# Performance work log

Hardware: AMD Instinct MI355X
Metric: run time of the kernel (lower is better)

Reference implementation:

```python
import jax, jax.numpy as jnp
import numpy as np

B, N, L = 1, 128, 256
D_MSA, D_HID, D_PAIR = 256, 32, 128
EPS = 1e-5


def setup_inputs() -> dict:
    key = jax.random.key(0)
    ks = jax.random.split(key, 8)
    msa = jax.random.normal(ks[0], (B, N, L, D_MSA), dtype=jnp.float32)
    pair = jax.random.normal(ks[1], (B, L, L, D_PAIR), dtype=jnp.float32)
    symmids = jax.random.randint(ks[2], (1,), 0, 1, dtype=jnp.int64)
    symmsub = jax.random.randint(ks[3], (1,), 0, 1, dtype=jnp.int64)
    # learned params (lecun-normal-ish scale = 1/sqrt(fan_in))
    ln_gamma = jnp.ones((D_MSA,), jnp.float32)
    ln_beta = jnp.zeros((D_MSA,), jnp.float32)
    w_left = jax.random.normal(ks[4], (D_MSA, D_HID), jnp.float32) / np.sqrt(D_MSA)
    b_left = jnp.zeros((D_HID,), jnp.float32)
    w_right = jax.random.normal(ks[5], (D_MSA, D_HID), jnp.float32) / np.sqrt(D_MSA)
    b_right = jnp.zeros((D_HID,), jnp.float32)
    w_out = jax.random.normal(ks[6], (D_HID * D_HID, D_PAIR), jnp.float32) / np.sqrt(D_HID * D_HID)
    b_out = jnp.zeros((D_PAIR,), jnp.float32)
    return {
        "msa": msa, "pair": pair, "symmids": symmids, "symmsub": symmsub,
        "ln_gamma": ln_gamma, "ln_beta": ln_beta,
        "w_left": w_left, "b_left": b_left,
        "w_right": w_right, "b_right": b_right,
        "w_out": w_out, "b_out": b_out,
    }


def reference(msa, pair, symmids, symmsub, ln_gamma, ln_beta,
              w_left, b_left, w_right, b_right, w_out, b_out):
    b, n, l, _ = msa.shape
    # LayerNorm over d_msa (biased variance, matching torch)
    mu = jnp.mean(msa, axis=-1, keepdims=True)
    var = jnp.mean(jnp.square(msa - mu), axis=-1, keepdims=True)
    x = (msa - mu) * jax.lax.rsqrt(var + EPS) * ln_gamma + ln_beta
    left = x @ w_left + b_left                       # [b, n, l, d_h]
    right = (x @ w_right + b_right) / float(n)       # [b, n, l, d_h]
    # outer product, reduced over MSA (s) dim -> [b, l, m, d_h, d_h]
    out = jnp.einsum('bsli,bsmj->blmij', left, right).reshape(b, l, l, -1)
    out = out @ w_out + b_out                        # [b, l, l, d_pair]
    return pair + out
```

## Files before the change

kernel.cpp:

```cpp
#include <hip/hip_runtime.h>


typedef float v4f __attribute__((ext_vector_type(4)));
typedef short v8s __attribute__((ext_vector_type(8)));

static __device__ inline unsigned short f2bf(float x) {
    unsigned int u = __builtin_bit_cast(unsigned int, x);
    return (unsigned short)((u + 0x7fffu + ((u >> 16) & 1u)) >> 16);
}

__global__ __launch_bounds__(256) void k_prep(const float* __restrict__ w_out,
                                              const float* __restrict__ wl,
                                              const float* __restrict__ wr,
                                              unsigned short* __restrict__ w2,
                                              unsigned short* __restrict__ wTg) {
    const int b = blockIdx.x, t = threadIdx.x;
    unsigned short tmp[8];
    if (b < 64) {
        int tgt = b * 2048 + t * 8;
        int p = (tgt >> 6) & 127;
        int ck = tgt >> 13, kc0 = tgt & 63;
        for (int e = 0; e < 8; ++e) {
            int kp = ck * 64 + kc0 + e;
            int j1 = (kp >> 9) & 1, qd = (kp >> 7) & 3, lp = (kp >> 3) & 15;
            int i1 = (kp >> 2) & 1, r = kp & 3;
            int ii = i1 * 16 + qd * 4 + r, jj = j1 * 16 + lp;
            tmp[e] = f2bf(w_out[(ii * 32 + jj) * 128 + p]);
        }
        *(uint4*)&w2[tgt] = *(const uint4*)tmp;
    } else {
        int tgt = (b - 64) * 2048 + t * 8;
        int c = tgt >> 8, d0 = tgt & 255;
        const float* src = (c < 32) ? wl : wr;
        int cc = c & 31;
        for (int e = 0; e < 8; ++e) tmp[e] = f2bf(src[(d0 + e) * 32 + cc]);
        *(uint4*)&wTg[tgt] = *(const uint4*)tmp;
    }
}

__global__ __launch_bounds__(256) void k_lnproj(
    const float* __restrict__ msa, const float* __restrict__ gamma, const float* __restrict__ beta,
    const unsigned short* __restrict__ wTg, const float* __restrict__ bl, const float* __restrict__ br,
    unsigned short* __restrict__ leftT, unsigned short* __restrict__ rightT) {
    __shared__ unsigned short xb[32 * 264];
    __shared__ unsigned short wlds[64 * 264];
    __shared__ unsigned short outT[64 * 40];

    const int t = threadIdx.x, lane = t & 63, w = t >> 6;
    const int l = blockIdx.x, s0 = blockIdx.y * 32;
    const int quad = lane >> 4, l15 = lane & 15;

    for (int it = 0; it < 8; ++it) {
        int idx = it * 2048 + t * 8;
        *(uint4*)&wlds[(idx >> 8) * 264 + (idx & 255)] = *(const uint4*)&wTg[idx];
    }

    float4 g4 = *(const float4*)&gamma[lane * 4];
    float4 be4 = *(const float4*)&beta[lane * 4];
    float4 vr[8]; float s1[8], s2[8];
    for (int r = 0; r < 8; ++r) {
        const float* row = msa + (size_t)((s0 + w * 8 + r) * 256 + l) * 256;
        vr[r] = *(const float4*)&row[lane * 4];
    }
    for (int r = 0; r < 8; ++r) {
        float4 v = vr[r];
        s1[r] = v.x + v.y + v.z + v.w;
        s2[r] = v.x * v.x + v.y * v.y + v.z * v.z + v.w * v.w;
    }
    for (int o = 32; o > 0; o >>= 1)
        for (int r = 0; r < 8; ++r) { s1[r] += __shfl_xor(s1[r], o); s2[r] += __shfl_xor(s2[r], o); }
    for (int r = 0; r < 8; ++r) {
        float mu = s1[r] * (1.f / 256);
        float rs = rsqrtf(s2[r] * (1.f / 256) - mu * mu + 1e-5f);
        float4 v = vr[r];
        ushort4 xs;
        xs.x = f2bf((v.x - mu) * rs * g4.x + be4.x);
        xs.y = f2bf((v.y - mu) * rs * g4.y + be4.y);
        xs.z = f2bf((v.z - mu) * rs * g4.z + be4.z);
        xs.w = f2bf((v.w - mu) * rs * g4.w + be4.w);
        *(ushort4*)&xb[(w * 8 + r) * 264 + lane * 4] = xs;
    }
    __syncthreads();

    const int mt = w >> 1, ntb = (w & 1) * 2;
    v4f acc[2] = {};
    const int frow = (mt * 16 + l15) * 264;
    for (int ks = 0; ks < 8; ++ks) {
        int k = ks * 32 + quad * 8;
        v8s a = *(const v8s*)&xb[frow + k];
        v8s b0 = *(const v8s*)&wlds[(ntb * 16 + l15) * 264 + k];
        v8s b1 = *(const v8s*)&wlds[((ntb + 1) * 16 + l15) * 264 + k];
        acc[0] = __builtin_amdgcn_mfma_f32_16x16x32_bf16(a, b0, acc[0], 0, 0, 0);
        acc[1] = __builtin_amdgcn_mfma_f32_16x16x32_bf16(a, b1, acc[1], 0, 0, 0);
    }

    for (int tn = 0; tn < 2; ++tn) {
        int c = (ntb + tn) * 16 + l15;
        float bias = c < 32 ? bl[c] : br[c - 32];
        float scale = c < 32 ? 1.f : (1.f / 128);
        for (int r = 0; r < 4; ++r)
            outT[c * 40 + mt * 16 + quad * 4 + r] = f2bf((acc[tn][r] + bias) * scale);
    }
    __syncthreads();

    {
        int c = t >> 2, q = t & 3;
        uint4 vv = *(const uint4*)&outT[c * 40 + q * 8];
        int kh = s0 >> 6;
        int g = ((s0 & 32) >> 3) + q;
        int g2 = g ^ (c & 7);
        unsigned short* dst = (c < 32) ? (leftT + l * 4096 + c * 128)
                                       : (rightT + l * 4096 + (c - 32) * 128);
        *(uint4*)&dst[kh * 64 + g2 * 8] = vv;
    }
}

__global__ __launch_bounds__(256) void k_outer(
    const unsigned short* __restrict__ leftT, const unsigned short* __restrict__ rightT,
    const unsigned short* __restrict__ w2g, const float* __restrict__ bout,
    const float* __restrict__ pairIn, float* __restrict__ out) {
    __shared__ alignas(16) unsigned short smem[24576];
    unsigned short* Ah = smem;
    unsigned short* Bh = smem + 8192;
    unsigned short* Obuf = smem;
    unsigned short* wbuf = smem + 16384;

    const int t = threadIdx.x, lane = t & 63, w = t >> 6;
    const int l0 = blockIdx.x * 4, m0 = blockIdx.y * 4;
    const int wm = w & 1, wn = w >> 1;
    const int quad = lane >> 4, l15 = lane & 15;

    const unsigned short* Asrc = leftT + l0 * 4096;
    const unsigned short* Bsrc = rightT + m0 * 4096;

    v4f acc[4][4] = {};
    for (int kh = 0; kh < 2; ++kh) {
        __syncthreads();
        for (int it = 0; it < 4; ++it) {
            int el = (it * 256 + t) * 8;
            int m = el >> 6, off = el & 63;
            *(uint4*)&Ah[m * 64 + off] = *(const uint4*)&Asrc[m * 128 + kh * 64 + off];
            *(uint4*)&Bh[m * 64 + off] = *(const uint4*)&Bsrc[m * 128 + kh * 64 + off];
        }
        __syncthreads();
        for (int ks = 0; ks < 2; ++ks) {
            int g = ks * 4 + quad;
            v8s a[4], bb[4];
            for (int i = 0; i < 4; ++i)
                a[i] = *(const v8s*)&Ah[(wm * 64 + i * 16 + l15) * 64 + ((g ^ (l15 & 7)) << 3)];
            for (int j = 0; j < 4; ++j)
                bb[j] = *(const v8s*)&Bh[(wn * 64 + j * 16 + l15) * 64 + ((g ^ (l15 & 7)) << 3)];
            for (int i = 0; i < 4; ++i)
                for (int j = 0; j < 4; ++j)
                    acc[i][j] = __builtin_amdgcn_mfma_f32_16x16x32_bf16(a[i], bb[j], acc[i][j], 0, 0, 0);
        }
    }
    __syncthreads();

    for (int a2 = 0; a2 < 2; ++a2)
        for (int b2 = 0; b2 < 2; ++b2) {
            int pr = (wm * 2 + a2) * 4 + wn * 2 + b2;
            for (int j1 = 0; j1 < 2; ++j1) {
                unsigned short tmp8[8];
                for (int i1 = 0; i1 < 2; ++i1)
                    for (int r = 0; r < 4; ++r)
                        tmp8[i1 * 4 + r] = f2bf(acc[a2 * 2 + i1][b2 * 2 + j1][r]);
                int pg = (j1 * 64 + lane) ^ (pr & 7);
                *(uint4*)&Obuf[pr * 1024 + pg * 8] = *(const uint4*)tmp8;
            }
        }
    __syncthreads();

    v4f acc2[2] = {};
    {
        const unsigned short* wsrc = w2g + w * 2048;
        unsigned short* wb = wbuf + w * 2048;
        int wa[4];
        uint4 pf[4];
        for (int u = 0; u < 4; ++u) {
            int g2 = (lane & 1) * 4 + u;
            wa[u] = (lane >> 1) * 64 + ((g2 ^ ((lane >> 1) & 7)) << 3);
            pf[u] = *(const uint4*)&wsrc[lane * 32 + u * 8];
        }
        for (int ck = 0; ck < 16; ++ck) {
            for (int u = 0; u < 4; ++u) *(uint4*)&wb[wa[u]] = pf[u];
            if (ck < 15)
                for (int u = 0; u < 4; ++u)
                    pf[u] = *(const uint4*)&wsrc[(ck + 1) * 8192 + lane * 32 + u * 8];
            for (int inner = 0; inner < 2; ++inner) {
                int g = ck * 8 + inner * 4 + quad;
                v8s a = *(const v8s*)&Obuf[l15 * 1024 + ((g ^ (l15 & 7)) << 3)];
                for (int tt = 0; tt < 2; ++tt) {
                    v8s bfr = *(const v8s*)&wb[(tt * 16 + l15) * 64 + (((inner * 4 + quad) ^ (l15 & 7)) << 3)];
                    acc2[tt] = __builtin_amdgcn_mfma_f32_16x16x32_bf16(a, bfr, acc2[tt], 0, 0, 0);
                }
            }
        }
    }

    for (int tt = 0; tt < 2; ++tt) {
        int p = (w * 2 + tt) * 16 + l15;
        float bo = bout[p];
        for (int r = 0; r < 4; ++r) {
            int pr = quad * 4 + r;
            int dl = pr >> 2, dm = pr & 3;
            size_t idx = (size_t)((l0 + dl) * 256 + (m0 + dm)) * 128 + p;
            out[idx] = pairIn[idx] + bo + acc2[tt][r];
        }
    }
}

extern "C" void kernel_launch(void* const* d_in, const int* in_sizes, int n_in,
                              void* d_out, int out_size, void* d_ws, size_t ws_size,
                              hipStream_t stream) {
    const float* msa   = (const float*)d_in[0];
    const float* pairI = (const float*)d_in[1];
    const float* gamma = (const float*)d_in[4];
    const float* beta  = (const float*)d_in[5];
    const float* wl    = (const float*)d_in[6];
    const float* bl    = (const float*)d_in[7];
    const float* wr    = (const float*)d_in[8];
    const float* br    = (const float*)d_in[9];
    const float* wout  = (const float*)d_in[10];
    const float* bout  = (const float*)d_in[11];
    float* out = (float*)d_out;

    unsigned short* leftT  = (unsigned short*)d_ws;
    unsigned short* rightT = leftT + 256 * 32 * 128;
    unsigned short* w2     = rightT + 256 * 32 * 128;
    unsigned short* wTg    = w2 + 131072;

    k_prep<<<dim3(72), 256, 0, stream>>>(wout, wl, wr, w2, wTg);
    k_lnproj<<<dim3(256, 4), 256, 0, stream>>>(msa, gamma, beta, wTg, bl, br, leftT, rightT);
    k_outer<<<dim3(64, 64), 256, 0, stream>>>(leftT, rightT, w2, bout, pairI, out);
}
```

Baseline: 200.7 us.

## Load weight fragments directly from global and use async global-to-LDS copies

In the LN+projection kernel, the staging of the projection weights through shared memory is removed, and MFMA B-fragments are read straight from global (L2-cached) memory. In the outer-product kernel, the A/B tile loads use global_load_lds to bypass registers. The w_out fragments are double-buffered in registers instead of being staged through LDS, which cuts LDS use from 48KB to 32KB and may raise occupancy. Risks: more global load latency exposed in the inner loops, and any mismatch between the w2g layout and the new direct fragment indexing.

```diff
diff --git a/kernel.cpp b/kernel.cpp
--- a/kernel.cpp
+++ b/kernel.cpp
@@ -7,6 +7,12 @@
 static __device__ inline unsigned short f2bf(float x) {
     unsigned int u = __builtin_bit_cast(unsigned int, x);
     return (unsigned short)((u + 0x7fffu + ((u >> 16) & 1u)) >> 16);
+}
+
+static __device__ inline void glds16(const void* g, void* l) {
+    __builtin_amdgcn_global_load_lds(
+        (const __attribute__((address_space(1))) unsigned int*)g,
+        (__attribute__((address_space(3))) unsigned int*)l, 16, 0, 0);
 }
 
 __global__ __launch_bounds__(256) void k_prep(const float* __restrict__ w_out,
@@ -43,17 +49,11 @@
     const unsigned short* __restrict__ wTg, const float* __restrict__ bl, const float* __restrict__ br,
     unsigned short* __restrict__ leftT, unsigned short* __restrict__ rightT) {
     __shared__ unsigned short xb[32 * 264];
-    __shared__ unsigned short wlds[64 * 264];
     __shared__ unsigned short outT[64 * 40];
 
     const int t = threadIdx.x, lane = t & 63, w = t >> 6;
     const int l = blockIdx.x, s0 = blockIdx.y * 32;
     const int quad = lane >> 4, l15 = lane & 15;
-
-    for (int it = 0; it < 8; ++it) {
-        int idx = it * 2048 + t * 8;
-        *(uint4*)&wlds[(idx >> 8) * 264 + (idx & 255)] = *(const uint4*)&wTg[idx];
-    }
 
     float4 g4 = *(const float4*)&gamma[lane * 4];
     float4 be4 = *(const float4*)&beta[lane * 4];
@@ -85,11 +85,12 @@
     const int mt = w >> 1, ntb = (w & 1) * 2;
     v4f acc[2] = {};
     const int frow = (mt * 16 + l15) * 264;
+    const int brow0 = (ntb * 16 + l15) * 256, brow1 = ((ntb + 1) * 16 + l15) * 256;
     for (int ks = 0; ks < 8; ++ks) {
         int k = ks * 32 + quad * 8;
         v8s a = *(const v8s*)&xb[frow + k];
-        v8s b0 = *(const v8s*)&wlds[(ntb * 16 + l15) * 264 + k];
-        v8s b1 = *(const v8s*)&wlds[((ntb + 1) * 16 + l15) * 264 + k];
+        v8s b0 = *(const v8s*)&wTg[brow0 + k];
+        v8s b1 = *(const v8s*)&wTg[brow1 + k];
         acc[0] = __builtin_amdgcn_mfma_f32_16x16x32_bf16(a, b0, acc[0], 0, 0, 0);
         acc[1] = __builtin_amdgcn_mfma_f32_16x16x32_bf16(a, b1, acc[1], 0, 0, 0);
     }
@@ -119,11 +120,10 @@
     const unsigned short* __restrict__ leftT, const unsigned short* __restrict__ rightT,
     const unsigned short* __restrict__ w2g, const float* __restrict__ bout,
     const float* __restrict__ pairIn, float* __restrict__ out) {
-    __shared__ alignas(16) unsigned short smem[24576];
+    __shared__ alignas(16) unsigned short smem[16384];
     unsigned short* Ah = smem;
     unsigned short* Bh = smem + 8192;
     unsigned short* Obuf = smem;
-    unsigned short* wbuf = smem + 16384;
 
     const int t = threadIdx.x, lane = t & 63, w = t >> 6;
     const int l0 = blockIdx.x * 4, m0 = blockIdx.y * 4;
@@ -137,10 +137,10 @@
     for (int kh = 0; kh < 2; ++kh) {
         __syncthreads();
         for (int it = 0; it < 4; ++it) {
-            int el = (it * 256 + t) * 8;
+            int el = it * 2048 + w * 512 + lane * 8;
             int m = el >> 6, off = el & 63;
-            *(uint4*)&Ah[m * 64 + off] = *(const uint4*)&Asrc[m * 128 + kh * 64 + off];
-            *(uint4*)&Bh[m * 64 + off] = *(const uint4*)&Bsrc[m * 128 + kh * 64 + off];
+            glds16(&Asrc[m * 128 + kh * 64 + off], &Ah[it * 2048 + w * 512]);
+            glds16(&Bsrc[m * 128 + kh * 64 + off], &Bh[it * 2048 + w * 512]);
         }
         __syncthreads();
         for (int ks = 0; ks < 2; ++ks) {
@@ -173,27 +173,27 @@
 
     v4f acc2[2] = {};
     {
-        const unsigned short* wsrc = w2g + w * 2048;
-        unsigned short* wb = wbuf + w * 2048;
-        int wa[4];
-        uint4 pf[4];
-        for (int u = 0; u < 4; ++u) {
-            int g2 = (lane & 1) * 4 + u;
-            wa[u] = (lane >> 1) * 64 + ((g2 ^ ((lane >> 1) & 7)) << 3);
-            pf[u] = *(const uint4*)&wsrc[lane * 32 + u * 8];
+        const int prow0 = ((w * 2) * 16 + l15) * 64;
+        const int prow1 = ((w * 2 + 1) * 16 + l15) * 64;
+        v8s bf[2][4];
+        for (int inner = 0; inner < 2; ++inner) {
+            bf[0][inner * 2 + 0] = *(const v8s*)&w2g[prow0 + inner * 32 + quad * 8];
+            bf[0][inner * 2 + 1] = *(const v8s*)&w2g[prow1 + inner * 32 + quad * 8];
         }
         for (int ck = 0; ck < 16; ++ck) {
-            for (int u = 0; u < 4; ++u) *(uint4*)&wb[wa[u]] = pf[u];
-            if (ck < 15)
-                for (int u = 0; u < 4; ++u)
-                    pf[u] = *(const uint4*)&wsrc[(ck + 1) * 8192 + lane * 32 + u * 8];
+            int cur = ck & 1, nxt = cur ^ 1;
+            if (ck < 15) {
+                const unsigned short* wc = w2g + (ck + 1) * 8192;
+                for (int inner = 0; inner < 2; ++inner) {
+                    bf[nxt][inner * 2 + 0] = *(const v8s*)&wc[prow0 + inner * 32 + quad * 8];
+                    bf[nxt][inner * 2 + 1] = *(const v8s*)&wc[prow1 + inner * 32 + quad * 8];
+                }
+            }
             for (int inner = 0; inner < 2; ++inner) {
                 int g = ck * 8 + inner * 4 + quad;
                 v8s a = *(const v8s*)&Obuf[l15 * 1024 + ((g ^ (l15 & 7)) << 3)];
-                for (int tt = 0; tt < 2; ++tt) {
-                    v8s bfr = *(const v8s*)&wb[(tt * 16 + l15) * 64 + (((inner * 4 + quad) ^ (l15 & 7)) << 3)];
-                    acc2[tt] = __builtin_amdgcn_mfma_f32_16x16x32_bf16(a, bfr, acc2[tt], 0, 0, 0);
-                }
+                acc2[0] = __builtin_amdgcn_mfma_f32_16x16x32_bf16(a, bf[cur][inner * 2 + 0], acc2[0], 0, 0, 0);
+                acc2[1] = __builtin_amdgcn_mfma_f32_16x16x32_bf16(a, bf[cur][inner * 2 + 1], acc2[1], 0, 0, 0);
             }
         }
     }
```

After: 255.3 us. +27.2%, slower.

## Enlarge outer-product tile to 4x8 residue pairs per block with register-staged loads

Applied to the files above, without the earlier changes.

Each k_outer block now covers 4 l by 8 m residues instead of 4x4, doubling B-side smem and accumulator tiles so the w_out projection weights are streamed once per 32 pairs rather than 16. Global loads for A/B are first staged into registers before a barrier, then written to shared memory. This halves grid size and w2 reloads, at the cost of more registers (acc[4][8]), 80KB dynamic shared memory and lower occupancy.

```diff
diff --git a/kernel.cpp b/kernel.cpp
--- a/kernel.cpp
+++ b/kernel.cpp
@@ -115,63 +115,69 @@
     }
 }
 
-__global__ __launch_bounds__(256) void k_outer(
+__global__ __launch_bounds__(256, 2) void k_outer(
     const unsigned short* __restrict__ leftT, const unsigned short* __restrict__ rightT,
     const unsigned short* __restrict__ w2g, const float* __restrict__ bout,
     const float* __restrict__ pairIn, float* __restrict__ out) {
-    __shared__ alignas(16) unsigned short smem[24576];
+    extern __shared__ unsigned short smem[];
     unsigned short* Ah = smem;
     unsigned short* Bh = smem + 8192;
     unsigned short* Obuf = smem;
-    unsigned short* wbuf = smem + 16384;
+    unsigned short* wbuf = smem + 32768;
 
     const int t = threadIdx.x, lane = t & 63, w = t >> 6;
-    const int l0 = blockIdx.x * 4, m0 = blockIdx.y * 4;
+    const int l0 = blockIdx.x * 4, m0 = blockIdx.y * 8;
     const int wm = w & 1, wn = w >> 1;
     const int quad = lane >> 4, l15 = lane & 15;
 
     const unsigned short* Asrc = leftT + l0 * 4096;
     const unsigned short* Bsrc = rightT + m0 * 4096;
 
-    v4f acc[4][4] = {};
+    v4f acc[4][8] = {};
     for (int kh = 0; kh < 2; ++kh) {
-        __syncthreads();
+        uint4 ra[4], rb[8];
         for (int it = 0; it < 4; ++it) {
             int el = (it * 256 + t) * 8;
             int m = el >> 6, off = el & 63;
-            *(uint4*)&Ah[m * 64 + off] = *(const uint4*)&Asrc[m * 128 + kh * 64 + off];
-            *(uint4*)&Bh[m * 64 + off] = *(const uint4*)&Bsrc[m * 128 + kh * 64 + off];
-        }
+            ra[it] = *(const uint4*)&Asrc[m * 128 + kh * 64 + off];
+        }
+        for (int it = 0; it < 8; ++it) {
+            int el = (it * 256 + t) * 8;
+            int m = el >> 6, off = el & 63;
+            rb[it] = *(const uint4*)&Bsrc[m * 128 + kh * 64 + off];
+        }
+        __syncthreads();
+        for (int it = 0; it < 4; ++it) *(uint4*)&Ah[(it * 256 + t) * 8] = ra[it];
+        for (int it = 0; it < 8; ++it) *(uint4*)&Bh[(it * 256 + t) * 8] = rb[it];
         __syncthreads();
         for (int ks = 0; ks < 2; ++ks) {
             int g = ks * 4 + quad;
-            v8s a[4], bb[4];
+            v8s a[4], bb[8];
             for (int i = 0; i < 4; ++i)
                 a[i] = *(const v8s*)&Ah[(wm * 64 + i * 16 + l15) * 64 + ((g ^ (l15 & 7)) << 3)];
-            for (int j = 0; j < 4; ++j)
-                bb[j] = *(const v8s*)&Bh[(wn * 64 + j * 16 + l15) * 64 + ((g ^ (l15 & 7)) << 3)];
+            for (int j = 0; j < 8; ++j)
+                bb[j] = *(const v8s*)&Bh[(wn * 128 + j * 16 + l15) * 64 + ((g ^ (l15 & 7)) << 3)];
             for (int i = 0; i < 4; ++i)
-                for (int j = 0; j < 4; ++j)
+                for (int j = 0; j < 8; ++j)
                     acc[i][j] = __builtin_amdgcn_mfma_f32_16x16x32_bf16(a[i], bb[j], acc[i][j], 0, 0, 0);
         }
     }
     __syncthreads();
 
     for (int a2 = 0; a2 < 2; ++a2)
-        for (int b2 = 0; b2 < 2; ++b2) {
-            int pr = (wm * 2 + a2) * 4 + wn * 2 + b2;
-            for (int j1 = 0; j1 < 2; ++j1) {
-                unsigned short tmp8[8];
-                for (int i1 = 0; i1 < 2; ++i1)
-                    for (int r = 0; r < 4; ++r)
-                        tmp8[i1 * 4 + r] = f2bf(acc[a2 * 2 + i1][b2 * 2 + j1][r]);
-                int pg = (j1 * 64 + lane) ^ (pr & 7);
-                *(uint4*)&Obuf[pr * 1024 + pg * 8] = *(const uint4*)tmp8;
-            }
-        }
-    __syncthreads();
-
-    v4f acc2[2] = {};
+        for (int j = 0; j < 8; ++j) {
+            int pr = (wm * 2 + a2) * 8 + wn * 4 + (j >> 1);
+            int j1 = j & 1;
+            unsigned short tmp8[8];
+            for (int i1 = 0; i1 < 2; ++i1)
+                for (int r = 0; r < 4; ++r)
+                    tmp8[i1 * 4 + r] = f2bf(acc[a2 * 2 + i1][j][r]);
+            int pg = (j1 * 64 + lane) ^ (pr & 7);
+            *(uint4*)&Obuf[pr * 1024 + pg * 8] = *(const uint4*)tmp8;
+        }
+    __syncthreads();
+
+    v4f acc2[2][2] = {};
     {
         const unsigned short* wsrc = w2g + w * 2048;
         unsigned short* wb = wbuf + w * 2048;
@@ -189,25 +195,29 @@
                     pf[u] = *(const uint4*)&wsrc[(ck + 1) * 8192 + lane * 32 + u * 8];
             for (int inner = 0; inner < 2; ++inner) {
                 int g = ck * 8 + inner * 4 + quad;
-                v8s a = *(const v8s*)&Obuf[l15 * 1024 + ((g ^ (l15 & 7)) << 3)];
+                int goff = ((g ^ (l15 & 7)) << 3);
+                v8s a0 = *(const v8s*)&Obuf[l15 * 1024 + goff];
+                v8s a1 = *(const v8s*)&Obuf[(16 + l15) * 1024 + goff];
                 for (int tt = 0; tt < 2; ++tt) {
                     v8s bfr = *(const v8s*)&wb[(tt * 16 + l15) * 64 + (((inner * 4 + quad) ^ (l15 & 7)) << 3)];
-                    acc2[tt] = __builtin_amdgcn_mfma_f32_16x16x32_bf16(a, bfr, acc2[tt], 0, 0, 0);
+                    acc2[0][tt] = __builtin_amdgcn_mfma_f32_16x16x32_bf16(a0, bfr, acc2[0][tt], 0, 0, 0);
+                    acc2[1][tt] = __builtin_amdgcn_mfma_f32_16x16x32_bf16(a1, bfr, acc2[1][tt], 0, 0, 0);
                 }
             }
         }
     }
 
-    for (int tt = 0; tt < 2; ++tt) {
-        int p = (w * 2 + tt) * 16 + l15;
-        float bo = bout[p];
-        for (int r = 0; r < 4; ++r) {
-            int pr = quad * 4 + r;
-            int dl = pr >> 2, dm = pr & 3;
-            size_t idx = (size_t)((l0 + dl) * 256 + (m0 + dm)) * 128 + p;
-            out[idx] = pairIn[idx] + bo + acc2[tt][r];
-        }
-    }
+    for (int mt = 0; mt < 2; ++mt)
+        for (int tt = 0; tt < 2; ++tt) {
+            int p = w * 32 + tt * 16 + l15;
+            float bo = bout[p];
+            for (int r = 0; r < 4; ++r) {
+                int pr = mt * 16 + quad * 4 + r;
+                int dl = pr >> 3, dm = pr & 7;
+                size_t idx = (size_t)((l0 + dl) * 256 + (m0 + dm)) * 128 + p;
+                out[idx] = pairIn[idx] + bo + acc2[mt][tt][r];
+            }
+        }
 }
 
 extern "C" void kernel_launch(void* const* d_in, const int* in_sizes, int n_in,
@@ -230,7 +240,10 @@
     unsigned short* w2     = rightT + 256 * 32 * 128;
     unsigned short* wTg    = w2 + 131072;
 
+    hipFuncSetAttribute(reinterpret_cast<const void*>(k_outer),
+                        hipFuncAttributeMaxDynamicSharedMemorySize, 81920);
+
     k_prep<<<dim3(72), 256, 0, stream>>>(wout, wl, wr, w2, wTg);
     k_lnproj<<<dim3(256, 4), 256, 0, stream>>>(msa, gamma, beta, wTg, bl, br, leftT, rightT);
-    k_outer<<<dim3(64, 64), 256, 0, stream>>>(leftT, rightT, w2, bout, pairI, out);
-}
+    k_outer<<<dim3(64, 32), 256, 81920, stream>>>(leftT, rightT, w2, bout, pairI, out);
+}
```

Result: slower. 231.9 us (+15.5%).
